# Performance work log

Measured on AMD Instinct MI355X. Metric: run time of the kernel, lower is better.

The kernel has to match this reference:

```python
import jax, jax.numpy as jnp
import numpy as np

EMBED_DIM = 1024
NUM_HEADS = 16
HEAD_DIM = EMBED_DIM // NUM_HEADS
B, S = 2, 2048


def setup_inputs() -> dict:
    key = jax.random.key(0)
    ks = jax.random.split(key, 5)
    scale = 1.0 / np.sqrt(EMBED_DIM)
    return {
        "inputs": jax.random.normal(ks[0], (B, S, EMBED_DIM), dtype=jnp.float32),
        "Wq": jax.random.normal(ks[1], (EMBED_DIM, EMBED_DIM), dtype=jnp.float32) * scale,
        "bq": jnp.zeros((EMBED_DIM,), dtype=jnp.float32),
        "Wk": jax.random.normal(ks[2], (EMBED_DIM, EMBED_DIM), dtype=jnp.float32) * scale,
        "bk": jnp.zeros((EMBED_DIM,), dtype=jnp.float32),
        "Wv": jax.random.normal(ks[3], (EMBED_DIM, EMBED_DIM), dtype=jnp.float32) * scale,
        "bv": jnp.zeros((EMBED_DIM,), dtype=jnp.float32),
        "Wo": jax.random.normal(ks[4], (EMBED_DIM, EMBED_DIM), dtype=jnp.float32) * scale,
        "bo": jnp.zeros((EMBED_DIM,), dtype=jnp.float32),
    }


def _split_heads(x):
    # [B, S, E] -> [B, H, S, Dh]
    b, s, _ = x.shape
    return x.reshape(b, s, NUM_HEADS, HEAD_DIM).transpose(0, 2, 1, 3)


def reference(inputs, Wq, bq, Wk, bk, Wv, bv, Wo, bo):
    q = _split_heads(inputs @ Wq + bq)  # [B, H, S, Dh]
    k = _split_heads(inputs @ Wk + bk)
    v = _split_heads(inputs @ Wv + bv)
    scale = 1.0 / jnp.sqrt(jnp.asarray(HEAD_DIM, dtype=q.dtype))
    scores = jnp.einsum("bhqd,bhkd->bhqk", q, k) * scale  # [B, H, S, S]
    weights = jax.nn.softmax(scores, axis=-1)
    attn = jnp.einsum("bhqk,bhkd->bhqd", weights, v)  # [B, H, S, Dh]
    concat = attn.transpose(0, 2, 1, 3).reshape(inputs.shape[0], -1, EMBED_DIM)
    return concat @ Wo + bo
```

## Files before the change

kernel.cpp:

```cpp
#include <hip/hip_runtime.h>


#define QSCALE 0.18033688011112042f

using bf16x8 = __attribute__((ext_vector_type(8))) short;
using f32x16 = __attribute__((ext_vector_type(16))) float;
using u16x8  = __attribute__((ext_vector_type(8))) unsigned short;

__device__ __forceinline__ unsigned short f2bf(float f) {
  unsigned int u = __float_as_uint(f);
  u += 0x7fffu + ((u >> 16) & 1u);
  return (unsigned short)(u >> 16);
}

__device__ __forceinline__ void gload_lds16(const unsigned short* g, unsigned short* l) {
  __builtin_amdgcn_global_load_lds(
      (const __attribute__((address_space(1))) unsigned int*)g,
      (__attribute__((address_space(3))) unsigned int*)l, 16, 0, 0);
}

__global__ void conv_x_kernel(const float* __restrict__ x, unsigned short* __restrict__ y) {
  int i = blockIdx.x * blockDim.x + threadIdx.x;
  const float4* xf = (const float4*)x;
  float4 a = xf[i * 2], b = xf[i * 2 + 1];
  u16x8 o;
  o[0] = f2bf(a.x); o[1] = f2bf(a.y); o[2] = f2bf(a.z); o[3] = f2bf(a.w);
  o[4] = f2bf(b.x); o[5] = f2bf(b.y); o[6] = f2bf(b.z); o[7] = f2bf(b.w);
  *((u16x8*)y + i) = o;
}

__global__ void conv_wT_kernel(const float* __restrict__ W0, const float* __restrict__ W1,
                               const float* __restrict__ W2, const float* __restrict__ W3,
                               unsigned short* __restrict__ out) {
  __shared__ float t[32][33];
  int z = blockIdx.z;
  const float* W = (z == 0) ? W0 : (z == 1) ? W1 : (z == 2) ? W2 : W3;
  unsigned short* o = out + (size_t)z * 1024 * 1024;
  int kt = blockIdx.y * 32, nt = blockIdx.x * 32;
  int tx = threadIdx.x, ty = threadIdx.y;
#pragma unroll
  for (int i = 0; i < 4; ++i)
    t[ty + i * 8][tx] = W[(size_t)(kt + ty + i * 8) * 1024 + nt + tx];
  __syncthreads();
#pragma unroll
  for (int i = 0; i < 4; ++i)
    o[(size_t)(nt + ty + i * 8) * 1024 + kt + tx] = f2bf(t[tx][ty + i * 8]);
}

__global__ __launch_bounds__(256) void gemm_bt_kernel(
    const unsigned short* __restrict__ A, const unsigned short* __restrict__ Bt,
    int mode, const float* __restrict__ bias0, const float* __restrict__ bias1,
    const float* __restrict__ bias2, unsigned short* __restrict__ Qh,
    unsigned short* __restrict__ Kh, unsigned short* __restrict__ Vt,
    float* __restrict__ Out) {
  const int K = 1024;
  __shared__ unsigned short SMEM[16384];

  int n0 = blockIdx.x * 128, m0 = blockIdx.y * 128;
  int tid = threadIdx.x;
  int w = tid >> 6, lane = tid & 63, l31 = lane & 31, half = lane >> 5;
  int wm = w >> 1, wn = w & 1;

  f32x16 acc[2][2];
#pragma unroll
  for (int i = 0; i < 2; ++i)
#pragma unroll
    for (int j = 0; j < 2; ++j)
#pragma unroll
      for (int r = 0; r < 16; ++r) acc[i][j][r] = 0.f;

  int srow = lane >> 2;
  int gchunk = (lane & 3) ^ (srow & 3);
  const unsigned short* Ag = A + (size_t)(m0 + 32 * w + srow) * K + gchunk * 8;
  const unsigned short* Bg = Bt + (size_t)(n0 + 32 * w + srow) * K + gchunk * 8;
  unsigned short* Asw = &SMEM[w * 1024];
  unsigned short* Bsw = &SMEM[8192 + w * 1024];

#pragma unroll
  for (int j = 0; j < 2; ++j) {
    gload_lds16(Ag + (size_t)(16 * j) * K, Asw + j * 512);
    gload_lds16(Bg + (size_t)(16 * j) * K, Bsw + j * 512);
  }

  for (int it = 0; it < 32; ++it) {
    int cur = (it & 1) * 4096;
    __syncthreads();
    if (it + 1 < 32) {
      int nxt = ((it + 1) & 1) * 4096;
      int kk = (it + 1) * 32;
#pragma unroll
      for (int j = 0; j < 2; ++j) {
        gload_lds16(Ag + kk + (size_t)(16 * j) * K, Asw + nxt + j * 512);
        gload_lds16(Bg + kk + (size_t)(16 * j) * K, Bsw + nxt + j * 512);
      }
    }
    const unsigned short* Asl = &SMEM[cur];
    const unsigned short* Bsl = &SMEM[8192 + cur];
#pragma unroll
    for (int kc = 0; kc < 2; ++kc) {
      int ph = ((kc * 2 + half) ^ (l31 & 3)) * 8;
      bf16x8 af[2], bfr[2];
#pragma unroll
      for (int mt = 0; mt < 2; ++mt)
        af[mt] = *(bf16x8*)&Asl[(wm * 64 + mt * 32 + l31) * 32 + ph];
#pragma unroll
      for (int nt = 0; nt < 2; ++nt)
        bfr[nt] = *(bf16x8*)&Bsl[(wn * 64 + nt * 32 + l31) * 32 + ph];
#pragma unroll
      for (int mt = 0; mt < 2; ++mt)
#pragma unroll
        for (int nt = 0; nt < 2; ++nt)
          acc[mt][nt] = __builtin_amdgcn_mfma_f32_32x32x16_bf16(af[mt], bfr[nt], acc[mt][nt], 0, 0, 0);
    }
  }

  if (mode == 1) {
#pragma unroll
    for (int mt = 0; mt < 2; ++mt)
#pragma unroll
      for (int nt = 0; nt < 2; ++nt)
#pragma unroll
        for (int r = 0; r < 16; ++r) {
          int row = (r & 3) + 8 * (r >> 2) + 4 * half;
          int gm = m0 + wm * 64 + mt * 32 + row;
          int gn = n0 + wn * 64 + nt * 32 + l31;
          Out[(size_t)gm * 1024 + gn] = acc[mt][nt][r] + bias0[gn];
        }
    return;
  }

  int btype = blockIdx.x >> 3;
  if (btype < 2) {
    const float* bp = btype ? bias1 : bias0;
    unsigned short* dst = btype ? Kh : Qh;
    float sc = btype ? 1.0f : QSCALE;
#pragma unroll
    for (int mt = 0; mt < 2; ++mt)
#pragma unroll
      for (int nt = 0; nt < 2; ++nt)
#pragma unroll
        for (int r = 0; r < 16; ++r) {
          int row = (r & 3) + 8 * (r >> 2) + 4 * half;
          int gm = m0 + wm * 64 + mt * 32 + row;
          int gn = n0 + wn * 64 + nt * 32 + l31;
          int e = gn & 1023;
          float v = (acc[mt][nt][r] + bp[e]) * sc;
          int hh = e >> 6, d = e & 63;
          int bb = gm >> 11, s = gm & 2047;
          dst[(((size_t)(bb * 16 + hh)) * 2048 + s) * 64 + d] = f2bf(v);
        }
  } else {
    __syncthreads();
    unsigned short* T = SMEM;
#pragma unroll
    for (int mt = 0; mt < 2; ++mt)
#pragma unroll
      for (int nt = 0; nt < 2; ++nt)
#pragma unroll
        for (int r = 0; r < 16; ++r) {
          int row = (r & 3) + 8 * (r >> 2) + 4 * half;
          int sl = wm * 64 + mt * 32 + row;
          int dl = wn * 64 + nt * 32 + l31;
          int e = (n0 - 2048) + dl;
          float v = acc[mt][nt][r] + bias2[e];
          T[dl * 128 + (sl ^ ((dl & 15) << 3))] = f2bf(v);
        }
    __syncthreads();
    int bb = m0 >> 11, s0 = m0 & 2047;
    int h0 = (n0 - 2048) >> 6;
    int rr0 = tid >> 2, csub = tid & 3;
#pragma unroll
    for (int pass = 0; pass < 2; ++pass) {
      int rr = rr0 + 64 * pass;
      int hh = h0 + (rr >> 6), d = rr & 63;
      unsigned short* vrow = Vt + (((size_t)(bb * 16 + hh)) * 64 + d) * 2048 + s0;
#pragma unroll
      for (int c = 0; c < 4; ++c) {
        int cc = c * 4 + csub;
        uint4 val = *(uint4*)&T[rr * 128 + ((cc ^ (rr & 15)) * 8)];
        *(uint4*)&vrow[cc * 8] = val;
      }
    }
  }
}

__global__ __launch_bounds__(256, 2) void attn_kernel(
    const unsigned short* __restrict__ Qh, const unsigned short* __restrict__ Kh,
    const unsigned short* __restrict__ Vt, unsigned short* __restrict__ Ctx) {
  __shared__ __align__(16) unsigned short SM[32768];

  int qt = blockIdx.x, h = blockIdx.y, b = blockIdx.z;
  int tid = threadIdx.x;
  int w = tid >> 6, lane = tid & 63, l31 = lane & 31, half = lane >> 5;
  int l7 = l31 & 7;
  int mw = w & 1, kw = w >> 1;

  size_t bh = (size_t)(b * 16 + h);
  const unsigned short* Qb  = Qh + (bh * 2048 + (size_t)qt * 128) * 64;
  const unsigned short* Kbh = Kh + bh * 131072;
  const unsigned short* Vbh = Vt + bh * 131072;

  bf16x8 qf0[4], qf1[4];
#pragma unroll
  for (int kc = 0; kc < 4; ++kc) {
    qf0[kc] = *(const bf16x8*)&Qb[(size_t)(mw * 64 + l31) * 64 + kc * 16 + half * 8];
    qf1[kc] = *(const bf16x8*)&Qb[(size_t)(mw * 64 + 32 + l31) * 64 + kc * 16 + half * 8];
  }

  int r8 = lane >> 3, gc = (lane & 7) ^ r8;
  const unsigned short* gbase;
  int gstep; size_t segstep;
  if (w < 2) { gbase = Kbh + (size_t)(w * 1024 + r8) * 64 + gc * 8; gstep = 4096; segstep = 512; }
  else       { gbase = Vbh + (size_t)r8 * 2048 + (w - 2) * 1024 + gc * 8; gstep = 64; segstep = 16384; }
  unsigned short* lb = SM + w * 4096;

#pragma unroll
  for (int j = 0; j < 8; ++j) gload_lds16(gbase + j * segstep, lb + j * 512);
  gbase += gstep;

  f32x16 o00, o01, o10, o11;
#pragma unroll
  for (int r = 0; r < 16; ++r) { o00[r] = 0.f; o01[r] = 0.f; o10[r] = 0.f; o11[r] = 0.f; }
  float l0 = 0.f, l1 = 0.f;

  for (int i = 0; i < 16; ++i) {
    __syncthreads();
    if (i < 15) {
      unsigned short* nb = lb + (((i + 1) & 1) << 14);
#pragma unroll
      for (int j = 0; j < 8; ++j) gload_lds16(gbase + j * segstep, nb + j * 512);
      gbase += gstep;
    }
    const unsigned short* cur = SM + ((i & 1) << 14);
    const unsigned short* Ksw = cur + kw * 4096;
    const unsigned short* Vsw = cur + 8192 + kw * 4096;

    f32x16 s00, s01, s10, s11;
#pragma unroll
    for (int r = 0; r < 16; ++r) { s00[r] = 0.f; s01[r] = 0.f; s10[r] = 0.f; s11[r] = 0.f; }
    __builtin_amdgcn_s_setprio(1);
#pragma unroll
    for (int kc = 0; kc < 4; ++kc) {
      int ph = ((kc * 2 + half) ^ l7) * 8;
      bf16x8 kb0 = *(bf16x8*)&Ksw[l31 * 64 + ph];
      bf16x8 kb1 = *(bf16x8*)&Ksw[(32 + l31) * 64 + ph];
      s00 = __builtin_amdgcn_mfma_f32_32x32x16_bf16(kb0, qf0[kc], s00, 0, 0, 0);
      s01 = __builtin_amdgcn_mfma_f32_32x32x16_bf16(kb1, qf0[kc], s01, 0, 0, 0);
      s10 = __builtin_amdgcn_mfma_f32_32x32x16_bf16(kb0, qf1[kc], s10, 0, 0, 0);
      s11 = __builtin_amdgcn_mfma_f32_32x32x16_bf16(kb1, qf1[kc], s11, 0, 0, 0);
    }
    __builtin_amdgcn_s_setprio(0);

    bf16x8 U0[4], U1[4];
    auto smx = [&](const f32x16& sa, const f32x16& sb, float& lacc, bf16x8* U) {
      float pa[16], pb[16];
#pragma unroll
      for (int r = 0; r < 16; ++r) { pa[r] = exp2f(sa[r]); pb[r] = exp2f(sb[r]); }
      float t0 = 0.f, t1 = 0.f, t2 = 0.f, t3 = 0.f;
#pragma unroll
      for (int r = 0; r < 16; r += 4) {
        t0 += pa[r] + pb[r]; t1 += pa[r + 1] + pb[r + 1];
        t2 += pa[r + 2] + pb[r + 2]; t3 += pa[r + 3] + pb[r + 3];
      }
      lacc += (t0 + t1) + (t2 + t3);
      unsigned int own[16];
#pragma unroll
      for (int m = 0; m < 4; ++m)
#pragma unroll
        for (int p = 0; p < 2; ++p) {
          int r = 4 * m + 2 * p;
          unsigned int wa, wb;
          asm("v_cvt_pk_bf16_f32 %0, %1, %2" : "=v"(wa) : "v"(pa[r]), "v"(pa[r + 1]));
          asm("v_cvt_pk_bf16_f32 %0, %1, %2" : "=v"(wb) : "v"(pb[r]), "v"(pb[r + 1]));
          own[2 * m + p] = wa;
          own[2 * m + 8 + p] = wb;
        }
#pragma unroll
      for (int kc = 0; kc < 4; ++kc) {
        unsigned int a0 = own[4 * kc],     b0 = own[4 * kc + 2];
        unsigned int a1 = own[4 * kc + 1], b1 = own[4 * kc + 3];
        asm("v_permlane32_swap_b32 %0, %1" : "+v"(a0), "+v"(b0));
        asm("v_permlane32_swap_b32 %0, %1" : "+v"(a1), "+v"(b1));
        union { unsigned int u[4]; bf16x8 v; } Uu;
        Uu.u[0] = a0; Uu.u[1] = a1; Uu.u[2] = b0; Uu.u[3] = b1;
        U[kc] = Uu.v;
      }
    };
    smx(s00, s01, l0, U0);
    smx(s10, s11, l1, U1);

    __builtin_amdgcn_s_setprio(1);
#pragma unroll
    for (int kc = 0; kc < 4; ++kc) {
      int ph = ((kc * 2 + half) ^ l7) * 8;
      bf16x8 vb0 = *(bf16x8*)&Vsw[l31 * 64 + ph];
      bf16x8 vb1 = *(bf16x8*)&Vsw[(32 + l31) * 64 + ph];
      o00 = __builtin_amdgcn_mfma_f32_32x32x16_bf16(U0[kc], vb0, o00, 0, 0, 0);
      o01 = __builtin_amdgcn_mfma_f32_32x32x16_bf16(U0[kc], vb1, o01, 0, 0, 0);
      o10 = __builtin_amdgcn_mfma_f32_32x32x16_bf16(U1[kc], vb0, o10, 0, 0, 0);
      o11 = __builtin_amdgcn_mfma_f32_32x32x16_bf16(U1[kc], vb1, o11, 0, 0, 0);
    }
    __builtin_amdgcn_s_setprio(0);
  }

  float lw0 = l0 + __shfl_xor(l0, 32);
  float lw1 = l1 + __shfl_xor(l1, 32);
  __syncthreads();
  float* mrgO = (float*)SM;
  float* mrgL = (float*)SM + 8192;
  if (kw == 1) {
    auto dump = [&](const f32x16& a0, const f32x16& a1, float lw, int qg) {
      float* dst = mrgO + (mw * 2 + qg) * 2048 + lane * 32;
#pragma unroll
      for (int c = 0; c < 8; ++c) {
        float4 t;
        if (c < 4) t = make_float4(a0[4 * c], a0[4 * c + 1], a0[4 * c + 2], a0[4 * c + 3]);
        else       t = make_float4(a1[4 * (c - 4)], a1[4 * (c - 4) + 1], a1[4 * (c - 4) + 2], a1[4 * (c - 4) + 3]);
        *(float4*)&dst[(c ^ l7) * 4] = t;
      }
      if (half == 0) mrgL[(mw * 2 + qg) * 32 + l31] = lw;
    };
    dump(o00, o01, lw0, 0);
    dump(o10, o11, lw1, 1);
  }
  __syncthreads();
  if (kw == 0) {
    auto fin = [&](f32x16& a0, f32x16& a1, float lw, int qg) {
      const float* src = mrgO + (mw * 2 + qg) * 2048 + lane * 32;
#pragma unroll
      for (int c = 0; c < 8; ++c) {
        float4 t = *(const float4*)&src[(c ^ l7) * 4];
        if (c < 4) { a0[4 * c] += t.x; a0[4 * c + 1] += t.y; a0[4 * c + 2] += t.z; a0[4 * c + 3] += t.w; }
        else       { a1[4 * (c - 4)] += t.x; a1[4 * (c - 4) + 1] += t.y; a1[4 * (c - 4) + 2] += t.z; a1[4 * (c - 4) + 3] += t.w; }
      }
      lw += mrgL[(mw * 2 + qg) * 32 + l31];
      float inv = 1.0f / lw;
#pragma unroll
      for (int r = 0; r < 16; ++r) {
        int rmap = (r & 3) + 8 * (r >> 2) + 4 * half;
        float invr = __shfl(inv, rmap);
        size_t row = (size_t)(b * 2048 + qt * 128 + mw * 64 + qg * 32 + rmap);
        Ctx[row * 1024 + h * 64 + l31]      = f2bf(a0[r] * invr);
        Ctx[row * 1024 + h * 64 + 32 + l31] = f2bf(a1[r] * invr);
      }
    };
    fin(o00, o01, lw0, 0);
    fin(o10, o11, lw1, 1);
  }
}

extern "C" void kernel_launch(void* const* d_in, const int* in_sizes, int n_in,
                              void* d_out, int out_size, void* d_ws, size_t ws_size,
                              hipStream_t stream) {
  const float* X  = (const float*)d_in[0];
  const float* Wq = (const float*)d_in[1];
  const float* bq = (const float*)d_in[2];
  const float* Wk = (const float*)d_in[3];
  const float* bk = (const float*)d_in[4];
  const float* Wv = (const float*)d_in[5];
  const float* bv = (const float*)d_in[6];
  const float* Wo = (const float*)d_in[7];
  const float* bo = (const float*)d_in[8];

  if (ws_size < (size_t)48 * 1024 * 1024) return;

  char* ws = (char*)d_ws;
  unsigned short* Xbf = (unsigned short*)(ws);
  unsigned short* Wt  = (unsigned short*)(ws + ((size_t)8 << 20));
  unsigned short* Qh  = (unsigned short*)(ws + ((size_t)16 << 20));
  unsigned short* Kh  = (unsigned short*)(ws + ((size_t)24 << 20));
  unsigned short* Vt  = (unsigned short*)(ws + ((size_t)32 << 20));
  unsigned short* Ctx = (unsigned short*)(ws + ((size_t)40 << 20));
  unsigned short* WtO = Wt + (size_t)3 * 1024 * 1024;

  conv_x_kernel<<<2048, 256, 0, stream>>>(X, Xbf);
  conv_wT_kernel<<<dim3(32, 32, 4), dim3(32, 8), 0, stream>>>(Wq, Wk, Wv, Wo, Wt);
  gemm_bt_kernel<<<dim3(24, 32), 256, 0, stream>>>(Xbf, Wt, 0, bq, bk, bv, Qh, Kh, Vt, nullptr);
  attn_kernel<<<dim3(16, 16, 2), 256, 0, stream>>>(Qh, Kh, Vt, Ctx);
  gemm_bt_kernel<<<dim3(8, 32), 256, 0, stream>>>(Ctx, WtO, 1, bo, bo, bo, nullptr, nullptr, nullptr, (float*)d_out);
}
```

Before: 210.4 us.

## Load K/V fragments directly from global, drop LDS staging, compute row sums via MFMA

The attention kernel no longer stages K and V tiles through double-buffered LDS with global_load_lds and per-iteration barriers. Each wave now reads its K and V MFMA fragments straight from global memory (relying on L2/L1 reuse across waves) and splits the score computation into two halves to reduce live registers. Softmax denominators are accumulated with an extra MFMA against a ones vector instead of VALU reductions, and exp2/reciprocal use the fast intrinsics. This removes the LDS traffic and syncs but adds redundant global loads per wave, exposes their latency, and adds MFMA work.

```diff
diff --git a/kernel.cpp b/kernel.cpp
--- a/kernel.cpp
+++ b/kernel.cpp
@@ -187,7 +187,7 @@
 __global__ __launch_bounds__(256, 2) void attn_kernel(
     const unsigned short* __restrict__ Qh, const unsigned short* __restrict__ Kh,
     const unsigned short* __restrict__ Vt, unsigned short* __restrict__ Ctx) {
-  __shared__ __align__(16) unsigned short SM[32768];
+  __shared__ __align__(16) float MRG[12288];
 
   int qt = blockIdx.x, h = blockIdx.y, b = blockIdx.z;
   int tid = threadIdx.x;
@@ -196,9 +196,7 @@
   int mw = w & 1, kw = w >> 1;
 
   size_t bh = (size_t)(b * 16 + h);
-  const unsigned short* Qb  = Qh + (bh * 2048 + (size_t)qt * 128) * 64;
-  const unsigned short* Kbh = Kh + bh * 131072;
-  const unsigned short* Vbh = Vt + bh * 131072;
+  const unsigned short* Qb = Qh + (bh * 2048 + (size_t)qt * 128) * 64;
 
   bf16x8 qf0[4], qf1[4];
 #pragma unroll
@@ -207,109 +205,108 @@
     qf1[kc] = *(const bf16x8*)&Qb[(size_t)(mw * 64 + 32 + l31) * 64 + kc * 16 + half * 8];
   }
 
-  int r8 = lane >> 3, gc = (lane & 7) ^ r8;
-  const unsigned short* gbase;
-  int gstep; size_t segstep;
-  if (w < 2) { gbase = Kbh + (size_t)(w * 1024 + r8) * 64 + gc * 8; gstep = 4096; segstep = 512; }
-  else       { gbase = Vbh + (size_t)r8 * 2048 + (w - 2) * 1024 + gc * 8; gstep = 64; segstep = 16384; }
-  unsigned short* lb = SM + w * 4096;
-
-#pragma unroll
-  for (int j = 0; j < 8; ++j) gload_lds16(gbase + j * segstep, lb + j * 512);
-  gbase += gstep;
-
-  f32x16 o00, o01, o10, o11;
-#pragma unroll
-  for (int r = 0; r < 16; ++r) { o00[r] = 0.f; o01[r] = 0.f; o10[r] = 0.f; o11[r] = 0.f; }
-  float l0 = 0.f, l1 = 0.f;
+  const unsigned short* K0 = Kh + bh * 131072 + (size_t)(kw * 1024 + l31) * 64 + half * 8;
+  const unsigned short* K1 = K0 + 2048;
+  const unsigned short* V0 = Vt + bh * 131072 + (size_t)l31 * 2048 + kw * 1024 + half * 8;
+  const unsigned short* V1 = V0 + 65536;
+
+  bf16x8 ones;
+#pragma unroll
+  for (int j = 0; j < 8; ++j) ones[j] = (short)0x3F80;
+
+  f32x16 o00, o01, o10, o11, la0, la1;
+#pragma unroll
+  for (int r = 0; r < 16; ++r) {
+    o00[r] = 0.f; o01[r] = 0.f; o10[r] = 0.f; o11[r] = 0.f;
+    la0[r] = 0.f; la1[r] = 0.f;
+  }
+
+  auto smx = [&](const f32x16& sa, const f32x16& sb, bf16x8* U) {
+    unsigned int own[16];
+#pragma unroll
+    for (int m = 0; m < 4; ++m)
+#pragma unroll
+      for (int p = 0; p < 2; ++p) {
+        int r = 4 * m + 2 * p;
+        float a0 = __builtin_amdgcn_exp2f(sa[r]);
+        float a1 = __builtin_amdgcn_exp2f(sa[r + 1]);
+        float b0 = __builtin_amdgcn_exp2f(sb[r]);
+        float b1 = __builtin_amdgcn_exp2f(sb[r + 1]);
+        unsigned int wa, wb;
+        asm("v_cvt_pk_bf16_f32 %0, %1, %2" : "=v"(wa) : "v"(a0), "v"(a1));
+        asm("v_cvt_pk_bf16_f32 %0, %1, %2" : "=v"(wb) : "v"(b0), "v"(b1));
+        own[2 * m + p] = wa;
+        own[2 * m + 8 + p] = wb;
+      }
+#pragma unroll
+    for (int kc = 0; kc < 4; ++kc) {
+      unsigned int a0 = own[4 * kc],     b0 = own[4 * kc + 2];
+      unsigned int a1 = own[4 * kc + 1], b1 = own[4 * kc + 3];
+      asm("v_permlane32_swap_b32 %0, %1" : "+v"(a0), "+v"(b0));
+      asm("v_permlane32_swap_b32 %0, %1" : "+v"(a1), "+v"(b1));
+      union { unsigned int u[4]; bf16x8 v; } Uu;
+      Uu.u[0] = a0; Uu.u[1] = a1; Uu.u[2] = b0; Uu.u[3] = b1;
+      U[kc] = Uu.v;
+    }
+  };
 
   for (int i = 0; i < 16; ++i) {
-    __syncthreads();
-    if (i < 15) {
-      unsigned short* nb = lb + (((i + 1) & 1) << 14);
-#pragma unroll
-      for (int j = 0; j < 8; ++j) gload_lds16(gbase + j * segstep, nb + j * 512);
-      gbase += gstep;
-    }
-    const unsigned short* cur = SM + ((i & 1) << 14);
-    const unsigned short* Ksw = cur + kw * 4096;
-    const unsigned short* Vsw = cur + 8192 + kw * 4096;
-
-    f32x16 s00, s01, s10, s11;
-#pragma unroll
-    for (int r = 0; r < 16; ++r) { s00[r] = 0.f; s01[r] = 0.f; s10[r] = 0.f; s11[r] = 0.f; }
+    f32x16 s0, s1;
+#pragma unroll
+    for (int r = 0; r < 16; ++r) { s0[r] = 0.f; s1[r] = 0.f; }
     __builtin_amdgcn_s_setprio(1);
 #pragma unroll
     for (int kc = 0; kc < 4; ++kc) {
-      int ph = ((kc * 2 + half) ^ l7) * 8;
-      bf16x8 kb0 = *(bf16x8*)&Ksw[l31 * 64 + ph];
-      bf16x8 kb1 = *(bf16x8*)&Ksw[(32 + l31) * 64 + ph];
-      s00 = __builtin_amdgcn_mfma_f32_32x32x16_bf16(kb0, qf0[kc], s00, 0, 0, 0);
-      s01 = __builtin_amdgcn_mfma_f32_32x32x16_bf16(kb1, qf0[kc], s01, 0, 0, 0);
-      s10 = __builtin_amdgcn_mfma_f32_32x32x16_bf16(kb0, qf1[kc], s10, 0, 0, 0);
-      s11 = __builtin_amdgcn_mfma_f32_32x32x16_bf16(kb1, qf1[kc], s11, 0, 0, 0);
+      bf16x8 a0 = *(const bf16x8*)(K0 + kc * 16);
+      bf16x8 a1 = *(const bf16x8*)(K1 + kc * 16);
+      s0 = __builtin_amdgcn_mfma_f32_32x32x16_bf16(a0, qf0[kc], s0, 0, 0, 0);
+      s1 = __builtin_amdgcn_mfma_f32_32x32x16_bf16(a1, qf0[kc], s1, 0, 0, 0);
     }
     __builtin_amdgcn_s_setprio(0);
-
-    bf16x8 U0[4], U1[4];
-    auto smx = [&](const f32x16& sa, const f32x16& sb, float& lacc, bf16x8* U) {
-      float pa[16], pb[16];
-#pragma unroll
-      for (int r = 0; r < 16; ++r) { pa[r] = exp2f(sa[r]); pb[r] = exp2f(sb[r]); }
-      float t0 = 0.f, t1 = 0.f, t2 = 0.f, t3 = 0.f;
-#pragma unroll
-      for (int r = 0; r < 16; r += 4) {
-        t0 += pa[r] + pb[r]; t1 += pa[r + 1] + pb[r + 1];
-        t2 += pa[r + 2] + pb[r + 2]; t3 += pa[r + 3] + pb[r + 3];
-      }
-      lacc += (t0 + t1) + (t2 + t3);
-      unsigned int own[16];
-#pragma unroll
-      for (int m = 0; m < 4; ++m)
-#pragma unroll
-        for (int p = 0; p < 2; ++p) {
-          int r = 4 * m + 2 * p;
-          unsigned int wa, wb;
-          asm("v_cvt_pk_bf16_f32 %0, %1, %2" : "=v"(wa) : "v"(pa[r]), "v"(pa[r + 1]));
-          asm("v_cvt_pk_bf16_f32 %0, %1, %2" : "=v"(wb) : "v"(pb[r]), "v"(pb[r + 1]));
-          own[2 * m + p] = wa;
-          own[2 * m + 8 + p] = wb;
-        }
-#pragma unroll
-      for (int kc = 0; kc < 4; ++kc) {
-        unsigned int a0 = own[4 * kc],     b0 = own[4 * kc + 2];
-        unsigned int a1 = own[4 * kc + 1], b1 = own[4 * kc + 3];
-        asm("v_permlane32_swap_b32 %0, %1" : "+v"(a0), "+v"(b0));
-        asm("v_permlane32_swap_b32 %0, %1" : "+v"(a1), "+v"(b1));
-        union { unsigned int u[4]; bf16x8 v; } Uu;
-        Uu.u[0] = a0; Uu.u[1] = a1; Uu.u[2] = b0; Uu.u[3] = b1;
-        U[kc] = Uu.v;
-      }
-    };
-    smx(s00, s01, l0, U0);
-    smx(s10, s11, l1, U1);
-
+    bf16x8 U0[4];
+    smx(s0, s1, U0);
+
+    f32x16 s2, s3;
+#pragma unroll
+    for (int r = 0; r < 16; ++r) { s2[r] = 0.f; s3[r] = 0.f; }
     __builtin_amdgcn_s_setprio(1);
 #pragma unroll
     for (int kc = 0; kc < 4; ++kc) {
-      int ph = ((kc * 2 + half) ^ l7) * 8;
-      bf16x8 vb0 = *(bf16x8*)&Vsw[l31 * 64 + ph];
-      bf16x8 vb1 = *(bf16x8*)&Vsw[(32 + l31) * 64 + ph];
-      o00 = __builtin_amdgcn_mfma_f32_32x32x16_bf16(U0[kc], vb0, o00, 0, 0, 0);
-      o01 = __builtin_amdgcn_mfma_f32_32x32x16_bf16(U0[kc], vb1, o01, 0, 0, 0);
-      o10 = __builtin_amdgcn_mfma_f32_32x32x16_bf16(U1[kc], vb0, o10, 0, 0, 0);
-      o11 = __builtin_amdgcn_mfma_f32_32x32x16_bf16(U1[kc], vb1, o11, 0, 0, 0);
+      bf16x8 a0 = *(const bf16x8*)(K0 + kc * 16);
+      bf16x8 a1 = *(const bf16x8*)(K1 + kc * 16);
+      s2 = __builtin_amdgcn_mfma_f32_32x32x16_bf16(a0, qf1[kc], s2, 0, 0, 0);
+      s3 = __builtin_amdgcn_mfma_f32_32x32x16_bf16(a1, qf1[kc], s3, 0, 0, 0);
     }
     __builtin_amdgcn_s_setprio(0);
-  }
-
-  float lw0 = l0 + __shfl_xor(l0, 32);
-  float lw1 = l1 + __shfl_xor(l1, 32);
-  __syncthreads();
-  float* mrgO = (float*)SM;
-  float* mrgL = (float*)SM + 8192;
+
+    bf16x8 vb0[4], vb1[4];
+#pragma unroll
+    for (int kc = 0; kc < 4; ++kc) {
+      vb0[kc] = *(const bf16x8*)(V0 + kc * 16);
+      vb1[kc] = *(const bf16x8*)(V1 + kc * 16);
+    }
+    bf16x8 U1[4];
+    smx(s2, s3, U1);
+
+    __builtin_amdgcn_s_setprio(1);
+#pragma unroll
+    for (int kc = 0; kc < 4; ++kc) {
+      o00 = __builtin_amdgcn_mfma_f32_32x32x16_bf16(U0[kc], vb0[kc], o00, 0, 0, 0);
+      o01 = __builtin_amdgcn_mfma_f32_32x32x16_bf16(U0[kc], vb1[kc], o01, 0, 0, 0);
+      la0 = __builtin_amdgcn_mfma_f32_32x32x16_bf16(U0[kc], ones, la0, 0, 0, 0);
+      o10 = __builtin_amdgcn_mfma_f32_32x32x16_bf16(U1[kc], vb0[kc], o10, 0, 0, 0);
+      o11 = __builtin_amdgcn_mfma_f32_32x32x16_bf16(U1[kc], vb1[kc], o11, 0, 0, 0);
+      la1 = __builtin_amdgcn_mfma_f32_32x32x16_bf16(U1[kc], ones, la1, 0, 0, 0);
+    }
+    __builtin_amdgcn_s_setprio(0);
+
+    K0 += 4096; K1 += 4096; V0 += 64; V1 += 64;
+  }
+
+  float* mrgO = MRG;
+  float* mrgL = MRG + 8192;
   if (kw == 1) {
-    auto dump = [&](const f32x16& a0, const f32x16& a1, float lw, int qg) {
+    auto dump = [&](const f32x16& a0, const f32x16& a1, const f32x16& la, int qg) {
       float* dst = mrgO + (mw * 2 + qg) * 2048 + lane * 32;
 #pragma unroll
       for (int c = 0; c < 8; ++c) {
@@ -318,14 +315,18 @@
         else       t = make_float4(a1[4 * (c - 4)], a1[4 * (c - 4) + 1], a1[4 * (c - 4) + 2], a1[4 * (c - 4) + 3]);
         *(float4*)&dst[(c ^ l7) * 4] = t;
       }
-      if (half == 0) mrgL[(mw * 2 + qg) * 32 + l31] = lw;
+      float* dl = mrgL + (mw * 2 + qg) * 1024 + lane * 16;
+#pragma unroll
+      for (int c = 0; c < 4; ++c)
+        *(float4*)&dl[(c ^ (l7 & 3)) * 4] =
+            make_float4(la[4 * c], la[4 * c + 1], la[4 * c + 2], la[4 * c + 3]);
     };
-    dump(o00, o01, lw0, 0);
-    dump(o10, o11, lw1, 1);
+    dump(o00, o01, la0, 0);
+    dump(o10, o11, la1, 1);
   }
   __syncthreads();
   if (kw == 0) {
-    auto fin = [&](f32x16& a0, f32x16& a1, float lw, int qg) {
+    auto fin = [&](f32x16& a0, f32x16& a1, f32x16& la, int qg) {
       const float* src = mrgO + (mw * 2 + qg) * 2048 + lane * 32;
 #pragma unroll
       for (int c = 0; c < 8; ++c) {
@@ -333,19 +334,23 @@
         if (c < 4) { a0[4 * c] += t.x; a0[4 * c + 1] += t.y; a0[4 * c + 2] += t.z; a0[4 * c + 3] += t.w; }
         else       { a1[4 * (c - 4)] += t.x; a1[4 * (c - 4) + 1] += t.y; a1[4 * (c - 4) + 2] += t.z; a1[4 * (c - 4) + 3] += t.w; }
       }
-      lw += mrgL[(mw * 2 + qg) * 32 + l31];
-      float inv = 1.0f / lw;
+      const float* dl = mrgL + (mw * 2 + qg) * 1024 + lane * 16;
+#pragma unroll
+      for (int c = 0; c < 4; ++c) {
+        float4 t = *(const float4*)&dl[(c ^ (l7 & 3)) * 4];
+        la[4 * c] += t.x; la[4 * c + 1] += t.y; la[4 * c + 2] += t.z; la[4 * c + 3] += t.w;
+      }
 #pragma unroll
       for (int r = 0; r < 16; ++r) {
         int rmap = (r & 3) + 8 * (r >> 2) + 4 * half;
-        float invr = __shfl(inv, rmap);
+        float inv = __builtin_amdgcn_rcpf(la[r]);
         size_t row = (size_t)(b * 2048 + qt * 128 + mw * 64 + qg * 32 + rmap);
-        Ctx[row * 1024 + h * 64 + l31]      = f2bf(a0[r] * invr);
-        Ctx[row * 1024 + h * 64 + 32 + l31] = f2bf(a1[r] * invr);
+        Ctx[row * 1024 + h * 64 + l31]      = f2bf(a0[r] * inv);
+        Ctx[row * 1024 + h * 64 + 32 + l31] = f2bf(a1[r] * inv);
       }
     };
-    fin(o00, o01, lw0, 0);
-    fin(o10, o11, lw1, 1);
+    fin(o00, o01, la0, 0);
+    fin(o10, o11, la1, 1);
   }
 }
 
```

Result: slower. 245.6 us (+16.7%).
